# Performance work log

Measured on AMD Instinct MI355X. Metric: run time of the kernel, lower is better.

## Reference

```python
import jax, jax.numpy as jnp
import numpy as np

WS = 7  # window_size


def setup_inputs() -> dict:
    key = jax.random.key(0)
    ks = jax.random.split(key, 4)
    B, C, H, W = 4, 384, 56, 56
    NH = 12
    x = jax.random.normal(ks[0], (B, C, H, W), dtype=jnp.float32)
    # 1x1 conv weights act as per-pixel linear maps over channels
    w_qkv = jax.random.normal(ks[1], (3 * C, C), dtype=jnp.float32) * (C ** -0.5)
    b_qkv = jnp.zeros((3 * C,), dtype=jnp.float32)
    w_proj = jax.random.normal(ks[2], (C, C), dtype=jnp.float32) * (C ** -0.5)
    b_proj = jnp.zeros((C,), dtype=jnp.float32)
    rel_bias = jax.random.normal(ks[3], (NH, WS, WS), dtype=jnp.float32) * 0.02
    return {"x": x, "w_qkv": w_qkv, "b_qkv": b_qkv,
            "w_proj": w_proj, "b_proj": b_proj, "rel_bias": rel_bias}


def reference(x, w_qkv, b_qkv, w_proj, b_proj, rel_bias):
    # Neighborhood attention: each query (i,j) attends to a ws x ws window of
    # keys/values centered at (i,j); borders handled by replication padding
    # (ReplicationPad2d), with a learned relative position bias (nh, ws, ws).
    B, C, H, W = x.shape
    nh, ws, _ = rel_bias.shape
    hd = C // nh
    p = ws // 2
    scale = hd ** -0.5

    # qkv 1x1 conv -> (B, 3, nh, hd, H, W)
    qkv = jnp.einsum('oc,bchw->bohw', w_qkv, x) + b_qkv[None, :, None, None]
    qkv = qkv.reshape(B, 3, nh, hd, H, W)
    q, k, v = qkv[:, 0] * scale, qkv[:, 1], qkv[:, 2]

    pad = ((0, 0), (0, 0), (0, 0), (p, p), (p, p))
    k_pad = jnp.pad(k, pad, mode='edge')  # replication padding
    v_pad = jnp.pad(v, pad, mode='edge')

    # attention logits over the ws*ws window offsets: (B, nh, H, W, K)
    logits = jnp.stack(
        [jnp.einsum('bnchw,bnchw->bnhw', q, k_pad[..., di:di + H, dj:dj + W])
         for di in range(ws) for dj in range(ws)], axis=-1)
    logits = logits + rel_bias.reshape(nh, ws * ws)[None, :, None, None, :]
    attn = jax.nn.softmax(logits, axis=-1)  # (attn_drop is identity in eval)

    # value windows: (B, nh, K, hd, H, W)
    v_win = jnp.stack([v_pad[..., di:di + H, dj:dj + W]
                       for di in range(ws) for dj in range(ws)], axis=2)
    out = jnp.einsum('bnhwk,bnkchw->bnchw', attn, v_win).reshape(B, C, H, W)

    # output projection 1x1 conv (proj_drop is identity in eval)
    out = jnp.einsum('oc,bchw->bohw', w_proj, out) + b_proj[None, :, None, None]
    return out
```

## Files before the change

kernel.cpp:

```cpp
#include <hip/hip_runtime.h>
#include <hip/hip_bf16.h>
#include <hip/hip_fp16.h>

#define S_HW 3136
#define SP   3200
#define IMG_W 56
#define C_DIM 384
#define NH_DIM 12
#define QKV_C 1152

#define TB 16
#define HALO 22
#define NPX 484
#define PLANE_B 3880

typedef float f32x4 __attribute__((ext_vector_type(4)));
typedef short bf16x8 __attribute__((ext_vector_type(8)));
typedef _Float16 f16x2 __attribute__((ext_vector_type(2)));

__device__ __forceinline__ void gld_lds16(const void* g, void* lds) {
    __builtin_amdgcn_global_load_lds(
        (const __attribute__((address_space(1))) void*)g,
        (__attribute__((address_space(3))) void*)lds, 16, 0, 0);
}

__device__ __forceinline__ float u2f(unsigned int u) { return __uint_as_float(u); }
__device__ __forceinline__ unsigned int f2bf_bits(float f) {
    unsigned int u = __float_as_uint(f);
    u += 0x7FFF + ((u >> 16) & 1);
    return u >> 16;
}
__device__ __forceinline__ unsigned int f2h_bits(float f) {
    return (unsigned int)__half_as_ushort(__float2half(f));
}

__device__ __forceinline__ float pair_sum(float v) {
    int o = __builtin_amdgcn_update_dpp(0, __float_as_int(v), 0xB1, 0xF, 0xF, true);
    return v + __uint_as_float((unsigned int)o);
}

__global__ __launch_bounds__(256) void convert_w2_kernel(
    const float* __restrict__ a, int na, __hip_bfloat16* __restrict__ oa,
    const float* __restrict__ b, int nb, __hip_bfloat16* __restrict__ ob)
{
    int i = blockIdx.x * 256 + threadIdx.x;
    if (i < na) oa[i] = __float2bfloat16(a[i]);
    else if (i < na + nb) ob[i - na] = __float2bfloat16(b[i - na]);
}

__global__ __launch_bounds__(256) void transpose_convert_kernel(
    const float* __restrict__ x, __hip_bfloat16* __restrict__ xt)
{
    __shared__ float t[32][33];
    const int b = blockIdx.z;
    const int c0 = blockIdx.y * 32, s0 = blockIdx.x * 32;
    const int tid = threadIdx.x;

    const int lc = tid >> 3, ls = (tid & 7) * 4;
    float4 v = *reinterpret_cast<const float4*>(
        &x[((size_t)b * C_DIM + c0 + lc) * S_HW + s0 + ls]);
    t[lc][ls + 0] = v.x; t[lc][ls + 1] = v.y;
    t[lc][ls + 2] = v.z; t[lc][ls + 3] = v.w;
    __syncthreads();

    const int ws = tid >> 3, wc = (tid & 7) * 4;
    uint2 pk;
    pk.x = f2bf_bits(t[wc + 0][ws]) | (f2bf_bits(t[wc + 1][ws]) << 16);
    pk.y = f2bf_bits(t[wc + 2][ws]) | (f2bf_bits(t[wc + 3][ws]) << 16);
    *reinterpret_cast<uint2*>(
        &xt[((size_t)b * SP + s0 + ws) * C_DIM + c0 + wc]) = pk;
}

template <bool TRANS_OUT, int NF, typename OutT>
__global__ __launch_bounds__(256) void gemm_bf16_mfma(
    const __hip_bfloat16* __restrict__ A,
    const __hip_bfloat16* __restrict__ Bt,
    const float* __restrict__ bias,
    OutT* __restrict__ Y,
    int O, int K, float qscale, int qrows)
{
    constexpr int BN = NF * 32;
    __shared__ char smem[8192 + BN * 64];
    char* As = smem;
    char* Bs = smem + 8192;

    const int b   = blockIdx.z;
    const int m0  = blockIdx.y * 128;
    const int n0  = blockIdx.x * BN;
    const int tid = threadIdx.x;
    const int w = tid >> 6, l = tid & 63;
    const int wr = w >> 1, wc = w & 1;

    const int srow = l >> 2;
    const int skk  = (l & 3) * 8;

    const __hip_bfloat16* Bb = Bt + (size_t)b * SP * K;

    f32x4 acc[4][NF];
    #pragma unroll
    for (int i = 0; i < 4; ++i)
        #pragma unroll
        for (int j = 0; j < NF; ++j) {
            f32x4 z = {0.f, 0.f, 0.f, 0.f};
            acc[i][j] = z;
        }

    const int frow = l & 15;
    const int fk   = (l >> 4) * 16;

    for (int k0 = 0; k0 < K; k0 += 32) {
        #pragma unroll
        for (int j = 0; j < 2; ++j) {
            const int chunk = w * 2 + j;
            const int m = chunk * 16 + srow;
            gld_lds16(A + (size_t)(m0 + m) * K + k0 + skk, As + chunk * 1024);
        }
        if (NF == 4) {
            #pragma unroll
            for (int j = 0; j < 2; ++j) {
                const int chunk = w * 2 + j;
                const int m = chunk * 16 + srow;
                gld_lds16(Bb + (size_t)(n0 + m) * K + k0 + skk, Bs + chunk * 1024);
            }
        } else {
            const int m = w * 16 + srow;
            gld_lds16(Bb + (size_t)(n0 + m) * K + k0 + skk, Bs + w * 1024);
        }
        __syncthreads();
        bf16x8 af[4], bfr[NF];
        #pragma unroll
        for (int mi = 0; mi < 4; ++mi)
            af[mi] = *reinterpret_cast<const bf16x8*>(
                As + (wr * 64 + mi * 16 + frow) * 64 + fk);
        #pragma unroll
        for (int ni = 0; ni < NF; ++ni)
            bfr[ni] = *reinterpret_cast<const bf16x8*>(
                Bs + (wc * (NF * 16) + ni * 16 + frow) * 64 + fk);
        #pragma unroll
        for (int mi = 0; mi < 4; ++mi)
            #pragma unroll
            for (int ni = 0; ni < NF; ++ni)
                acc[mi][ni] = __builtin_amdgcn_mfma_f32_16x16x32_bf16(
                    af[mi], bfr[ni], acc[mi][ni], 0, 0, 0);
        __syncthreads();
    }

    const int crow0 = (l >> 4) * 4;
    const int ccol  = l & 15;
    if (TRANS_OUT) {
        __hip_bfloat16* Yb = (__hip_bfloat16*)Y + (size_t)b * SP * O;
        #pragma unroll
        for (int ni = 0; ni < NF; ++ni) {
            const int col = n0 + wc * (NF * 16) + ni * 16 + ccol;
            if (col >= S_HW) continue;
            #pragma unroll
            for (int mi = 0; mi < 4; ++mi) {
                const int row0 = m0 + wr * 64 + mi * 16 + crow0;
                const float sc = (row0 < qrows) ? qscale : 1.f;
                float v0 = (acc[mi][ni][0] + bias[row0 + 0]) * sc;
                float v1 = (acc[mi][ni][1] + bias[row0 + 1]) * sc;
                float v2 = (acc[mi][ni][2] + bias[row0 + 2]) * sc;
                float v3 = (acc[mi][ni][3] + bias[row0 + 3]) * sc;
                uint2 pk;
                pk.x = f2h_bits(v0) | (f2h_bits(v1) << 16);
                pk.y = f2h_bits(v2) | (f2h_bits(v3) << 16);
                *reinterpret_cast<uint2*>(&Yb[(size_t)col * O + row0]) = pk;
            }
        }
    } else {
        float* Yb = (float*)Y + (size_t)b * O * S_HW;
        #pragma unroll
        for (int ni = 0; ni < NF; ++ni) {
            const int col = n0 + wc * (NF * 16) + ni * 16 + ccol;
            if (col >= S_HW) continue;
            #pragma unroll
            for (int mi = 0; mi < 4; ++mi) {
                #pragma unroll
                for (int r = 0; r < 4; ++r) {
                    const int row = m0 + wr * 64 + mi * 16 + crow0 + r;
                    float v = acc[mi][ni][r] + bias[row];
                    if (row < qrows) v *= qscale;
                    Yb[(size_t)row * S_HW + col] = v;
                }
            }
        }
    }
}

__global__ __launch_bounds__(512) void na_attn_kernel(
    const __hip_bfloat16* __restrict__ qkvt, const float* __restrict__ rel_bias,
    __hip_bfloat16* __restrict__ outt)
{
    __shared__ alignas(16) char halo[8 * PLANE_B];

    const int blk  = blockIdx.x;
    const int tile = blk & 15;
    const int bn   = blk >> 4;
    const int nh   = bn % NH_DIM;
    const int b    = bn / NH_DIM;
    const int th0  = (tile >> 2) * TB;
    const int tw0  = (tile & 3) * TB;

    const int tid  = threadIdx.x;
    const int px   = tid >> 1;
    const int half = tid & 1;
    const int ty = px >> 4, tx = px & 15;
    const int h = th0 + ty, w = tw0 + tx;
    const bool valid = (h < 56) && (w < 56);
    const int s = h * IMG_W + w;

    const __hip_bfloat16* base = qkvt + (size_t)b * SP * QKV_C;
    const int co = nh * 32;
    const int pl0 = 4 * half;

    #pragma unroll
    for (int i = 0; i < 4; ++i) {
        const int idx = tid + i * 512;
        if (idx < NPX * 4) {
            const int p = idx >> 2, g = idx & 3;
            const int hy = p / HALO, hx = p - hy * HALO;
            const int y = min(max(th0 - 3 + hy, 0), 55);
            const int x = min(max(tw0 - 3 + hx, 0), 55);
            const uint4 v = *reinterpret_cast<const uint4*>(
                base + (size_t)(y * IMG_W + x) * QKV_C + C_DIM + co + g * 8);
            uint2 lo; lo.x = v.x; lo.y = v.y;
            uint2 hi; hi.x = v.z; hi.y = v.w;
            *reinterpret_cast<uint2*>(&halo[(2 * g + 0) * PLANE_B + p * 8]) = lo;
            *reinterpret_cast<uint2*>(&halo[(2 * g + 1) * PLANE_B + p * 8]) = hi;
        }
    }

    unsigned int qreg[8];
    if (valid) {
        const uint4* qp = reinterpret_cast<const uint4*>(
            base + (size_t)s * QKV_C + co + 16 * half);
        uint4 q0 = qp[0], q1 = qp[1];
        qreg[0] = q0.x; qreg[1] = q0.y; qreg[2] = q0.z; qreg[3] = q0.w;
        qreg[4] = q1.x; qreg[5] = q1.y; qreg[6] = q1.z; qreg[7] = q1.w;
    }
    __syncthreads();

    float logits[49];
    if (valid) {
        #pragma unroll
        for (int di = 0; di < 7; ++di) {
            #pragma unroll
            for (int dj = 0; dj < 7; ++dj) {
                const int hp = (ty + di) * HALO + (tx + dj);
                const char* hb = halo + hp * 8;
                float acc0 = 0.f, acc1 = 0.f;
                #pragma unroll
                for (int pl = 0; pl < 4; ++pl) {
                    uint2 kk = *reinterpret_cast<const uint2*>(
                        hb + (pl0 + pl) * PLANE_B);
#if __has_builtin(__builtin_amdgcn_fdot2)
                    acc0 = __builtin_amdgcn_fdot2(
                        __builtin_bit_cast(f16x2, qreg[2 * pl]),
                        __builtin_bit_cast(f16x2, kk.x), acc0, false);
                    acc1 = __builtin_amdgcn_fdot2(
                        __builtin_bit_cast(f16x2, qreg[2 * pl + 1]),
                        __builtin_bit_cast(f16x2, kk.y), acc1, false);
#else
                    f16x2 qa = __builtin_bit_cast(f16x2, qreg[2 * pl]);
                    f16x2 qb = __builtin_bit_cast(f16x2, qreg[2 * pl + 1]);
                    f16x2 ka = __builtin_bit_cast(f16x2, kk.x);
                    f16x2 kb = __builtin_bit_cast(f16x2, kk.y);
                    acc0 += (float)qa[0] * (float)ka[0] + (float)qa[1] * (float)ka[1];
                    acc1 += (float)qb[0] * (float)kb[0] + (float)qb[1] * (float)kb[1];
#endif
                }
                logits[di * 7 + dj] =
                    pair_sum(acc0 + acc1) + rel_bias[(nh * 7 + di) * 7 + dj];
            }
        }
    }
    __syncthreads();

    #pragma unroll
    for (int i = 0; i < 4; ++i) {
        const int idx = tid + i * 512;
        if (idx < NPX * 4) {
            const int p = idx >> 2, g = idx & 3;
            const int hy = p / HALO, hx = p - hy * HALO;
            const int y = min(max(th0 - 3 + hy, 0), 55);
            const int x = min(max(tw0 - 3 + hx, 0), 55);
            const uint4 v = *reinterpret_cast<const uint4*>(
                base + (size_t)(y * IMG_W + x) * QKV_C + 2 * C_DIM + co + g * 8);
            uint2 lo; lo.x = v.x; lo.y = v.y;
            uint2 hi; hi.x = v.z; hi.y = v.w;
            *reinterpret_cast<uint2*>(&halo[(2 * g + 0) * PLANE_B + p * 8]) = lo;
            *reinterpret_cast<uint2*>(&halo[(2 * g + 1) * PLANE_B + p * 8]) = hi;
        }
    }

    unsigned int ppk[25];
    float inv = 0.f;
    if (valid) {
        float mx = logits[0];
        #pragma unroll
        for (int i = 1; i < 49; ++i) mx = fmaxf(mx, logits[i]);
        float sum = 0.f;
        #pragma unroll
        for (int i = 0; i < 24; ++i) {
            float e0 = __expf(logits[2 * i] - mx);
            float e1 = __expf(logits[2 * i + 1] - mx);
            sum += e0 + e1;
            ppk[i] = f2bf_bits(e0) << 16 | f2bf_bits(e1);
        }
        {
            float e0 = __expf(logits[48] - mx);
            sum += e0;
            ppk[24] = f2bf_bits(e0) << 16;
        }
        inv = 1.f / sum;
    }
    __syncthreads();

    if (valid) {
        float o[16];
        #pragma unroll
        for (int c = 0; c < 16; ++c) o[c] = 0.f;

        #pragma unroll
        for (int n = 0; n < 49; ++n) {
            const unsigned int pu = ppk[n >> 1];
            const float pv = (n & 1) ? u2f(pu << 16) : u2f(pu & 0xFFFF0000u);
            const int di = n / 7, dj = n % 7;
            const int hp = (ty + di) * HALO + (tx + dj);
            const char* hb = halo + hp * 8;
            #pragma unroll
            for (int pl = 0; pl < 4; ++pl) {
                uint2 vv = *reinterpret_cast<const uint2*>(
                    hb + (pl0 + pl) * PLANE_B);
                f16x2 va = __builtin_bit_cast(f16x2, vv.x);
                f16x2 vb = __builtin_bit_cast(f16x2, vv.y);
                o[4 * pl + 0] = fmaf((float)va[0], pv, o[4 * pl + 0]);
                o[4 * pl + 1] = fmaf((float)va[1], pv, o[4 * pl + 1]);
                o[4 * pl + 2] = fmaf((float)vb[0], pv, o[4 * pl + 2]);
                o[4 * pl + 3] = fmaf((float)vb[1], pv, o[4 * pl + 3]);
            }
        }

        uint4* dst = reinterpret_cast<uint4*>(
            outt + ((size_t)b * SP + s) * C_DIM + co + 16 * half);
        #pragma unroll
        for (int g = 0; g < 2; ++g) {
            uint4 pk;
            pk.x = f2bf_bits(o[8 * g + 0] * inv) | (f2bf_bits(o[8 * g + 1] * inv) << 16);
            pk.y = f2bf_bits(o[8 * g + 2] * inv) | (f2bf_bits(o[8 * g + 3] * inv) << 16);
            pk.z = f2bf_bits(o[8 * g + 4] * inv) | (f2bf_bits(o[8 * g + 5] * inv) << 16);
            pk.w = f2bf_bits(o[8 * g + 6] * inv) | (f2bf_bits(o[8 * g + 7] * inv) << 16);
            dst[g] = pk;
        }
    }
}

extern "C" void kernel_launch(void* const* d_in, const int* in_sizes, int n_in,
                              void* d_out, int out_size, void* d_ws, size_t ws_size,
                              hipStream_t stream) {
    const float* x        = (const float*)d_in[0];
    const float* w_qkv    = (const float*)d_in[1];
    const float* b_qkv    = (const float*)d_in[2];
    const float* w_proj   = (const float*)d_in[3];
    const float* b_proj   = (const float*)d_in[4];
    const float* rel_bias = (const float*)d_in[5];
    float* out = (float*)d_out;

    __hip_bfloat16* xt   = (__hip_bfloat16*)d_ws;
    __hip_bfloat16* wq   = xt + (size_t)4 * SP * C_DIM;
    __hip_bfloat16* wp   = wq + (size_t)QKV_C * C_DIM;
    __hip_bfloat16* qkvt = wp + (size_t)C_DIM * C_DIM;
    __hip_bfloat16* att  = qkvt + (size_t)4 * SP * QKV_C;

    const float scale = 0.17677669529663687f;
    const int nwq = QKV_C * C_DIM, nwp = C_DIM * C_DIM;

    convert_w2_kernel<<<dim3((nwq + nwp + 255) / 256), 256, 0, stream>>>(
        w_qkv, nwq, wq, w_proj, nwp, wp);
    transpose_convert_kernel<<<dim3(98, 12, 4), dim3(256), 0, stream>>>(x, xt);

    gemm_bf16_mfma<true, 4, __hip_bfloat16><<<dim3(25, 9, 4), 256, 0, stream>>>(
        wq, xt, b_qkv, qkvt, QKV_C, C_DIM, scale, C_DIM);

    na_attn_kernel<<<dim3(4 * NH_DIM * 16), 512, 0, stream>>>(qkvt, rel_bias, att);

    gemm_bf16_mfma<false, 2, float><<<dim3(50, 3, 4), 256, 0, stream>>>(
        wp, att, b_proj, out, C_DIM, C_DIM, 1.f, 0);
}
```

Baseline: 104.3 us.

## Double GEMM k-step per barrier, interleave attention planes across half-threads, pad halo planes

The bf16 MFMA GEMM now loads two 32-wide K slices into separate LDS buffers per iteration and runs both MFMA batches between one pair of barriers. This halves the number of __syncthreads per K and doubles LDS use. The neighborhood-attention kernel changes which channel planes each thread pair reads: the two half-threads now alternate planes instead of each taking a contiguous half. The halo plane stride is padded to change LDS bank mapping, and launch_bounds(512,4) is added, which may cap registers and risk spills.

```diff
diff --git a/kernel.cpp b/kernel.cpp
--- a/kernel.cpp
+++ b/kernel.cpp
@@ -12,7 +12,7 @@
 #define TB 16
 #define HALO 22
 #define NPX 484
-#define PLANE_B 3880
+#define PLANE_B 3976
 
 typedef float f32x4 __attribute__((ext_vector_type(4)));
 typedef short bf16x8 __attribute__((ext_vector_type(8)));
@@ -80,9 +80,11 @@
     int O, int K, float qscale, int qrows)
 {
     constexpr int BN = NF * 32;
-    __shared__ char smem[8192 + BN * 64];
-    char* As = smem;
-    char* Bs = smem + 8192;
+    __shared__ char smem[16384 + BN * 128];
+    char* As0 = smem;
+    char* As1 = smem + 8192;
+    char* Bs0 = smem + 16384;
+    char* Bs1 = smem + 16384 + BN * 64;
 
     const int b   = blockIdx.z;
     const int m0  = blockIdx.y * 128;
@@ -108,40 +110,62 @@
     const int frow = l & 15;
     const int fk   = (l >> 4) * 16;
 
-    for (int k0 = 0; k0 < K; k0 += 32) {
+    for (int k0 = 0; k0 < K; k0 += 64) {
         #pragma unroll
         for (int j = 0; j < 2; ++j) {
             const int chunk = w * 2 + j;
             const int m = chunk * 16 + srow;
-            gld_lds16(A + (size_t)(m0 + m) * K + k0 + skk, As + chunk * 1024);
+            gld_lds16(A + (size_t)(m0 + m) * K + k0 + skk,      As0 + chunk * 1024);
+            gld_lds16(A + (size_t)(m0 + m) * K + k0 + 32 + skk, As1 + chunk * 1024);
         }
         if (NF == 4) {
             #pragma unroll
             for (int j = 0; j < 2; ++j) {
                 const int chunk = w * 2 + j;
                 const int m = chunk * 16 + srow;
-                gld_lds16(Bb + (size_t)(n0 + m) * K + k0 + skk, Bs + chunk * 1024);
+                gld_lds16(Bb + (size_t)(n0 + m) * K + k0 + skk,      Bs0 + chunk * 1024);
+                gld_lds16(Bb + (size_t)(n0 + m) * K + k0 + 32 + skk, Bs1 + chunk * 1024);
             }
         } else {
             const int m = w * 16 + srow;
-            gld_lds16(Bb + (size_t)(n0 + m) * K + k0 + skk, Bs + w * 1024);
+            gld_lds16(Bb + (size_t)(n0 + m) * K + k0 + skk,      Bs0 + w * 1024);
+            gld_lds16(Bb + (size_t)(n0 + m) * K + k0 + 32 + skk, Bs1 + w * 1024);
         }
         __syncthreads();
-        bf16x8 af[4], bfr[NF];
-        #pragma unroll
-        for (int mi = 0; mi < 4; ++mi)
-            af[mi] = *reinterpret_cast<const bf16x8*>(
-                As + (wr * 64 + mi * 16 + frow) * 64 + fk);
-        #pragma unroll
-        for (int ni = 0; ni < NF; ++ni)
-            bfr[ni] = *reinterpret_cast<const bf16x8*>(
-                Bs + (wc * (NF * 16) + ni * 16 + frow) * 64 + fk);
-        #pragma unroll
-        for (int mi = 0; mi < 4; ++mi)
+        {
+            bf16x8 af[4], bfr[NF];
+            #pragma unroll
+            for (int mi = 0; mi < 4; ++mi)
+                af[mi] = *reinterpret_cast<const bf16x8*>(
+                    As0 + (wr * 64 + mi * 16 + frow) * 64 + fk);
             #pragma unroll
             for (int ni = 0; ni < NF; ++ni)
-                acc[mi][ni] = __builtin_amdgcn_mfma_f32_16x16x32_bf16(
-                    af[mi], bfr[ni], acc[mi][ni], 0, 0, 0);
+                bfr[ni] = *reinterpret_cast<const bf16x8*>(
+                    Bs0 + (wc * (NF * 16) + ni * 16 + frow) * 64 + fk);
+            #pragma unroll
+            for (int mi = 0; mi < 4; ++mi)
+                #pragma unroll
+                for (int ni = 0; ni < NF; ++ni)
+                    acc[mi][ni] = __builtin_amdgcn_mfma_f32_16x16x32_bf16(
+                        af[mi], bfr[ni], acc[mi][ni], 0, 0, 0);
+        }
+        {
+            bf16x8 af[4], bfr[NF];
+            #pragma unroll
+            for (int mi = 0; mi < 4; ++mi)
+                af[mi] = *reinterpret_cast<const bf16x8*>(
+                    As1 + (wr * 64 + mi * 16 + frow) * 64 + fk);
+            #pragma unroll
+            for (int ni = 0; ni < NF; ++ni)
+                bfr[ni] = *reinterpret_cast<const bf16x8*>(
+                    Bs1 + (wc * (NF * 16) + ni * 16 + frow) * 64 + fk);
+            #pragma unroll
+            for (int mi = 0; mi < 4; ++mi)
+                #pragma unroll
+                for (int ni = 0; ni < NF; ++ni)
+                    acc[mi][ni] = __builtin_amdgcn_mfma_f32_16x16x32_bf16(
+                        af[mi], bfr[ni], acc[mi][ni], 0, 0, 0);
+        }
         __syncthreads();
     }
 
@@ -187,7 +211,7 @@
     }
 }
 
-__global__ __launch_bounds__(512) void na_attn_kernel(
+__global__ __launch_bounds__(512, 4) void na_attn_kernel(
     const __hip_bfloat16* __restrict__ qkvt, const float* __restrict__ rel_bias,
     __hip_bfloat16* __restrict__ outt)
 {
@@ -211,7 +235,6 @@
 
     const __hip_bfloat16* base = qkvt + (size_t)b * SP * QKV_C;
     const int co = nh * 32;
-    const int pl0 = 4 * half;
 
     #pragma unroll
     for (int i = 0; i < 4; ++i) {
@@ -232,11 +255,13 @@
 
     unsigned int qreg[8];
     if (valid) {
-        const uint4* qp = reinterpret_cast<const uint4*>(
-            base + (size_t)s * QKV_C + co + 16 * half);
-        uint4 q0 = qp[0], q1 = qp[1];
-        qreg[0] = q0.x; qreg[1] = q0.y; qreg[2] = q0.z; qreg[3] = q0.w;
-        qreg[4] = q1.x; qreg[5] = q1.y; qreg[6] = q1.z; qreg[7] = q1.w;
+        #pragma unroll
+        for (int j = 0; j < 4; ++j) {
+            uint2 qv = *reinterpret_cast<const uint2*>(
+                base + (size_t)s * QKV_C + co + 8 * j + 4 * half);
+            qreg[2 * j]     = qv.x;
+            qreg[2 * j + 1] = qv.y;
+        }
     }
     __syncthreads();
 
@@ -250,19 +275,19 @@
                 const char* hb = halo + hp * 8;
                 float acc0 = 0.f, acc1 = 0.f;
                 #pragma unroll
-                for (int pl = 0; pl < 4; ++pl) {
+                for (int j = 0; j < 4; ++j) {
                     uint2 kk = *reinterpret_cast<const uint2*>(
-                        hb + (pl0 + pl) * PLANE_B);
+                        hb + (2 * j + half) * PLANE_B);
 #if __has_builtin(__builtin_amdgcn_fdot2)
                     acc0 = __builtin_amdgcn_fdot2(
-                        __builtin_bit_cast(f16x2, qreg[2 * pl]),
+                        __builtin_bit_cast(f16x2, qreg[2 * j]),
                         __builtin_bit_cast(f16x2, kk.x), acc0, false);
                     acc1 = __builtin_amdgcn_fdot2(
-                        __builtin_bit_cast(f16x2, qreg[2 * pl + 1]),
+                        __builtin_bit_cast(f16x2, qreg[2 * j + 1]),
                         __builtin_bit_cast(f16x2, kk.y), acc1, false);
 #else
-                    f16x2 qa = __builtin_bit_cast(f16x2, qreg[2 * pl]);
-                    f16x2 qb = __builtin_bit_cast(f16x2, qreg[2 * pl + 1]);
+                    f16x2 qa = __builtin_bit_cast(f16x2, qreg[2 * j]);
+                    f16x2 qb = __builtin_bit_cast(f16x2, qreg[2 * j + 1]);
                     f16x2 ka = __builtin_bit_cast(f16x2, kk.x);
                     f16x2 kb = __builtin_bit_cast(f16x2, kk.y);
                     acc0 += (float)qa[0] * (float)ka[0] + (float)qa[1] * (float)ka[1];
@@ -329,28 +354,25 @@
             const int hp = (ty + di) * HALO + (tx + dj);
             const char* hb = halo + hp * 8;
             #pragma unroll
-            for (int pl = 0; pl < 4; ++pl) {
+            for (int j = 0; j < 4; ++j) {
                 uint2 vv = *reinterpret_cast<const uint2*>(
-                    hb + (pl0 + pl) * PLANE_B);
+                    hb + (2 * j + half) * PLANE_B);
                 f16x2 va = __builtin_bit_cast(f16x2, vv.x);
                 f16x2 vb = __builtin_bit_cast(f16x2, vv.y);
-                o[4 * pl + 0] = fmaf((float)va[0], pv, o[4 * pl + 0]);
-                o[4 * pl + 1] = fmaf((float)va[1], pv, o[4 * pl + 1]);
-                o[4 * pl + 2] = fmaf((float)vb[0], pv, o[4 * pl + 2]);
-                o[4 * pl + 3] = fmaf((float)vb[1], pv, o[4 * pl + 3]);
+                o[4 * j + 0] = fmaf((float)va[0], pv, o[4 * j + 0]);
+                o[4 * j + 1] = fmaf((float)va[1], pv, o[4 * j + 1]);
+                o[4 * j + 2] = fmaf((float)vb[0], pv, o[4 * j + 2]);
+                o[4 * j + 3] = fmaf((float)vb[1], pv, o[4 * j + 3]);
             }
         }
 
-        uint4* dst = reinterpret_cast<uint4*>(
-            outt + ((size_t)b * SP + s) * C_DIM + co + 16 * half);
-        #pragma unroll
-        for (int g = 0; g < 2; ++g) {
-            uint4 pk;
-            pk.x = f2bf_bits(o[8 * g + 0] * inv) | (f2bf_bits(o[8 * g + 1] * inv) << 16);
-            pk.y = f2bf_bits(o[8 * g + 2] * inv) | (f2bf_bits(o[8 * g + 3] * inv) << 16);
-            pk.z = f2bf_bits(o[8 * g + 4] * inv) | (f2bf_bits(o[8 * g + 5] * inv) << 16);
-            pk.w = f2bf_bits(o[8 * g + 6] * inv) | (f2bf_bits(o[8 * g + 7] * inv) << 16);
-            dst[g] = pk;
+        __hip_bfloat16* ob = outt + ((size_t)b * SP + s) * C_DIM + co + 4 * half;
+        #pragma unroll
+        for (int j = 0; j < 4; ++j) {
+            uint2 pk;
+            pk.x = f2bf_bits(o[4 * j + 0] * inv) | (f2bf_bits(o[4 * j + 1] * inv) << 16);
+            pk.y = f2bf_bits(o[4 * j + 2] * inv) | (f2bf_bits(o[4 * j + 3] * inv) << 16);
+            *reinterpret_cast<uint2*>(ob + 8 * j) = pk;
         }
     }
 }
```

After: 101.4 us. 1.03x faster.
